# Performance work log

Measured on AMD Instinct MI355X. Metric: run time of the kernel, lower is better.

## Reference

```python
import jax, jax.numpy as jnp
import numpy as np

N_NODES = 100000
IN_C, HID_C, OUT_C = 128, 128, 64
N_EDGES, N_POS, N_NEG = 1600000, 200000, 200000
BN_EPS = 1e-5


def setup_inputs() -> dict:
    key = jax.random.key(0)
    ks = jax.random.split(key, 24)
    s = 0.05
    inp = {
        'x': jax.random.normal(ks[0], (N_NODES, IN_C), jnp.float32),
        'edge_index': jax.random.randint(ks[1], (2, N_EDGES), 0, N_NODES, jnp.int64 if jax.config.jax_enable_x64 else jnp.int32),
        'pos_edge_index': jax.random.randint(ks[2], (2, N_POS), 0, N_NODES, jnp.int32),
        'neg_edge_index': jax.random.randint(ks[3], (2, N_NEG), 0, N_NODES, jnp.int32),
        # SAGEConv layer 1 (in->hid): lin_l (bias) on aggregated neighbors, lin_r (no bias) on root
        'Wl1': jax.random.normal(ks[4], (IN_C, HID_C), jnp.float32) * s,
        'bl1': jnp.zeros((HID_C,), jnp.float32),
        'Wr1': jax.random.normal(ks[5], (IN_C, HID_C), jnp.float32) * s,
        'g1': jnp.ones((HID_C,), jnp.float32),
        'b1': jnp.zeros((HID_C,), jnp.float32),
        # SAGEConv layer 2 (hid->hid)
        'Wl2': jax.random.normal(ks[6], (HID_C, HID_C), jnp.float32) * s,
        'bl2': jnp.zeros((HID_C,), jnp.float32),
        'Wr2': jax.random.normal(ks[7], (HID_C, HID_C), jnp.float32) * s,
        'g2': jnp.ones((HID_C,), jnp.float32),
        'b2': jnp.zeros((HID_C,), jnp.float32),
        # SAGEConv layer 3 (hid->out)
        'Wl3': jax.random.normal(ks[8], (HID_C, OUT_C), jnp.float32) * s,
        'bl3': jnp.zeros((OUT_C,), jnp.float32),
        'Wr3': jax.random.normal(ks[9], (HID_C, OUT_C), jnp.float32) * s,
        # edge predictor: Linear(2*out, hid) -> ReLU -> Linear(hid, 1)
        'We1': jax.random.normal(ks[10], (2 * OUT_C, HID_C), jnp.float32) * s,
        'be1': jnp.zeros((HID_C,), jnp.float32),
        'We2': jax.random.normal(ks[11], (HID_C, 1), jnp.float32) * s,
        'be2': jnp.zeros((1,), jnp.float32),
    }
    return inp


def _sage_conv(x, src, dst, Wl, bl, Wr):
    # mean aggregation of source features at destination nodes (PyG SAGEConv default)
    msg = x[src]                                                   # [E, C] gather
    agg = jax.ops.segment_sum(msg, dst, num_segments=N_NODES)      # [N, C] scatter-add
    deg = jax.ops.segment_sum(jnp.ones((src.shape[0],), x.dtype), dst, num_segments=N_NODES)
    mean = agg / jnp.maximum(deg, 1.0)[:, None]
    return mean @ Wl + bl + x @ Wr


def _bn_eval(x, gamma, beta):
    # BatchNorm1d eval mode with init running stats (mean 0, var 1)
    return x * (gamma / jnp.sqrt(1.0 + BN_EPS)) + beta


def _encode(x, edge_index, Wl1, bl1, Wr1, g1, b1, Wl2, bl2, Wr2, g2, b2, Wl3, bl3, Wr3):
    src, dst = edge_index[0], edge_index[1]
    h = x
    # layer 1 (+ residual: in_channels == hidden_channels)
    h1 = jax.nn.relu(_bn_eval(_sage_conv(h, src, dst, Wl1, bl1, Wr1), g1, b1))
    h = h1 + h if h.shape[1] == h1.shape[1] else h1
    # layer 2 (+ residual)
    h2 = jax.nn.relu(_bn_eval(_sage_conv(h, src, dst, Wl2, bl2, Wr2), g2, b2))
    h = h2 + h
    # output layer (no norm/relu/residual)
    return _sage_conv(h, src, dst, Wl3, bl3, Wr3)


def _decode(z, edge_index, We1, be1, We2, be2):
    s, d = edge_index[0], edge_index[1]
    ef = jnp.concatenate([z[s], z[d]], axis=-1)           # [E, 2*OUT_C]
    hidden = jax.nn.relu(ef @ We1 + be1)
    return jax.nn.sigmoid((hidden @ We2 + be2)[:, 0])


def reference(x, edge_index, pos_edge_index, neg_edge_index,
              Wl1, bl1, Wr1, g1, b1, Wl2, bl2, Wr2, g2, b2, Wl3, bl3, Wr3,
              We1, be1, We2, be2):
    z = _encode(x, edge_index, Wl1, bl1, Wr1, g1, b1, Wl2, bl2, Wr2, g2, b2, Wl3, bl3, Wr3)
    pos = _decode(z, pos_edge_index, We1, be1, We2, be2)
    neg = _decode(z, neg_edge_index, We1, be1, We2, be2)
    return (z, pos, neg)
```

## Files before the change

kernel.cpp:

```cpp
#include <hip/hip_runtime.h>
#include <hip/hip_bf16.h>

typedef unsigned short u16;
typedef unsigned char u8;
typedef short short8 __attribute__((ext_vector_type(8)));
typedef float floatx4 __attribute__((ext_vector_type(4)));
typedef float floatx2 __attribute__((ext_vector_type(2)));

__device__ __forceinline__ float b2f(u16 u) {
    unsigned v = ((unsigned)u) << 16;
    float f;
    __builtin_memcpy(&f, &v, 4);
    return f;
}
__device__ __forceinline__ float b2f_lo(unsigned w) { return b2f((u16)(w & 0xffffu)); }
__device__ __forceinline__ float b2f_hi(unsigned w) { return b2f((u16)(w >> 16)); }
__device__ __forceinline__ u16 f2b(float f) {
    unsigned u;
    __builtin_memcpy(&u, &f, 4);
    u = u + 0x7fffu + ((u >> 16) & 1u);
    return (u16)(u >> 16);
}
__device__ __forceinline__ unsigned pack2(float a, float b) {
    return (unsigned)f2b(a) | ((unsigned)f2b(b) << 16);
}
__device__ __forceinline__ float loadp(const void* p, int i, int f) {
    return f ? ((const float*)p)[i] : b2f(((const u16*)p)[i]);
}
__device__ __forceinline__ u8 f2e4m3(float v) {
    int r = __builtin_amdgcn_cvt_pk_fp8_f32(v, v, 0, false);
    return (u8)(r & 0xff);
}
__device__ __forceinline__ void acc16_fp8(float* a, uint4 p) {
    floatx2 f;
    f = __builtin_amdgcn_cvt_pk_f32_fp8((int)p.x, false); a[0] += f[0];  a[1] += f[1];
    f = __builtin_amdgcn_cvt_pk_f32_fp8((int)p.x, true);  a[2] += f[0];  a[3] += f[1];
    f = __builtin_amdgcn_cvt_pk_f32_fp8((int)p.y, false); a[4] += f[0];  a[5] += f[1];
    f = __builtin_amdgcn_cvt_pk_f32_fp8((int)p.y, true);  a[6] += f[0];  a[7] += f[1];
    f = __builtin_amdgcn_cvt_pk_f32_fp8((int)p.z, false); a[8] += f[0];  a[9] += f[1];
    f = __builtin_amdgcn_cvt_pk_f32_fp8((int)p.z, true);  a[10] += f[0]; a[11] += f[1];
    f = __builtin_amdgcn_cvt_pk_f32_fp8((int)p.w, false); a[12] += f[0]; a[13] += f[1];
    f = __builtin_amdgcn_cvt_pk_f32_fp8((int)p.w, true);  a[14] += f[0]; a[15] += f[1];
}

__global__ void sniff_kernel(const unsigned* __restrict__ xw, const int* __restrict__ eiw,
                             int* __restrict__ flags) {
    __shared__ int s_fp32, s_i64;
    if (threadIdx.x == 0) { s_fp32 = 0; s_i64 = 1; }
    __syncthreads();
    int t = threadIdx.x;
    unsigned w = xw[t];
    float lo = b2f_lo(w);
    if (!(fabsf(lo) <= 64.0f)) atomicOr(&s_fp32, 1);
    if (eiw[2 * t + 1] != 0) atomicAnd(&s_i64, 0);
    __syncthreads();
    if (t == 0) { flags[0] = s_fp32; flags[1] = s_i64; }
}

__global__ void cvt_x_kernel(const void* __restrict__ x, u16* __restrict__ xb,
                             u16* __restrict__ x8,
                             const int* __restrict__ flags, int nPairs) {
    int f = flags[0];
    int i = blockIdx.x * 256 + threadIdx.x;
    if (i >= nPairs) return;
    float lo, hi;
    if (f) {
        float2 v = ((const float2*)x)[i];
        lo = v.x; hi = v.y;
        ((unsigned*)xb)[i] = pack2(lo, hi);
    } else {
        unsigned w = ((const unsigned*)x)[i];
        lo = b2f_lo(w); hi = b2f_hi(w);
        ((unsigned*)xb)[i] = w;
    }
    int r = __builtin_amdgcn_cvt_pk_fp8_f32(lo, hi, 0, false);
    x8[i] = (u16)(r & 0xffff);
}

__global__ void prep_all_kernel(const void* Wl1, const void* Wr1, u16* __restrict__ Wcat1,
                                const void* Wl2, const void* Wr2, u16* __restrict__ Wcat2,
                                const void* Wl3, const void* Wr3, u16* __restrict__ Wcat3,
                                const void* We1, u16* __restrict__ Web,
                                const void* g1, const void* b1, const void* bl1,
                                float* __restrict__ al1, float* __restrict__ bt1,
                                const void* g2, const void* b2, const void* bl2,
                                float* __restrict__ al2, float* __restrict__ bt2,
                                const void* bl3,
                                float* __restrict__ al3, float* __restrict__ bt3,
                                const void* be1, const void* We2, const void* be2,
                                float* __restrict__ dparams,
                                const int* __restrict__ flags) {
    int f = flags[0];
    int idx = blockIdx.x * 256 + threadIdx.x;
    if (idx < 16384) {
        int k = idx >> 7, n = idx & 127;
        Wcat1[n * 256 + k]       = f ? f2b(((const float*)Wl1)[idx]) : ((const u16*)Wl1)[idx];
        Wcat1[n * 256 + 128 + k] = f ? f2b(((const float*)Wr1)[idx]) : ((const u16*)Wr1)[idx];
    } else if (idx < 32768) {
        int i = idx - 16384;
        int k = i >> 7, n = i & 127;
        Wcat2[n * 256 + k]       = f ? f2b(((const float*)Wl2)[i]) : ((const u16*)Wl2)[i];
        Wcat2[n * 256 + 128 + k] = f ? f2b(((const float*)Wr2)[i]) : ((const u16*)Wr2)[i];
    } else if (idx < 49152) {
        int i = idx - 32768;
        int k = i >> 7, n = i & 127;
        const void* src = (n < 64) ? Wl3 : Wr3;
        int j = k * 64 + (n & 63);
        Wcat3[n * 128 + k] = f ? f2b(((const float*)src)[j]) : ((const u16*)src)[j];
    } else if (idx < 65536) {
        int i = idx - 49152;
        int k = i >> 7, n = i & 127;
        Web[n * 128 + k] = f ? f2b(((const float*)We1)[i]) : ((const u16*)We1)[i];
    } else {
        int i = idx - 65536;
        if (i < 128) {
            float s = loadp(g1, i, f) * rsqrtf(1.0f + 1e-5f);
            al1[i] = s;
            bt1[i] = loadp(bl1, i, f) * s + loadp(b1, i, f);
        } else if (i < 256) {
            int j = i - 128;
            float s = loadp(g2, j, f) * rsqrtf(1.0f + 1e-5f);
            al2[j] = s;
            bt2[j] = loadp(bl2, j, f) * s + loadp(b2, j, f);
        } else if (i < 384) {
            int j = i - 256;
            al3[j] = 1.0f;
            bt3[j] = (j < 64) ? 0.0f : loadp(bl3, j - 64, f);
        } else if (i < 512) {
            int j = i - 384;
            dparams[j] = loadp(be1, j, f);
            dparams[128 + j] = loadp(We2, j, f);
            if (j == 0) dparams[256] = loadp(be2, 0, f);
        }
    }
}

__device__ __forceinline__ int edge_at(const int* ei, long long idx, int i64) {
    return i64 ? ei[2 * idx] : ei[idx];
}

__global__ __launch_bounds__(256) void bucket_count_kernel(const int* __restrict__ ei,
                                                           int* __restrict__ blockhist,
                                                           int E, int EPB, int B1, int nbuck,
                                                           const int* __restrict__ flags) {
    __shared__ int hist[1024];
    for (int i = threadIdx.x; i < nbuck; i += 256) hist[i] = 0;
    __syncthreads();
    int i64 = flags[1];
    int b = blockIdx.x;
    int lo = b * EPB, hi = min(lo + EPB, E);
    for (int e = lo + (int)threadIdx.x; e < hi; e += 256) {
        int d = edge_at(ei, (long long)E + e, i64);
        atomicAdd(&hist[d >> 7], 1);
    }
    __syncthreads();
    for (int k = threadIdx.x; k < nbuck; k += 256)
        blockhist[(size_t)k * B1 + b] = hist[k];
}

__global__ __launch_bounds__(64) void colscan_kernel(int* __restrict__ blockhist,
                                                     int* __restrict__ coltot, int B1) {
    int k = blockIdx.x, l = threadIdx.x;
    int* bh = blockhist + (size_t)k * B1;
    int x0 = (l < B1) ? bh[l] : 0;
    int x1 = (64 + l < B1) ? bh[64 + l] : 0;
    int s0 = x0;
    #pragma unroll
    for (int off = 1; off < 64; off <<= 1) {
        int u = __shfl_up(s0, off, 64);
        if (l >= off) s0 += u;
    }
    int tot0 = __shfl(s0, 63, 64);
    int s1 = x1;
    #pragma unroll
    for (int off = 1; off < 64; off <<= 1) {
        int u = __shfl_up(s1, off, 64);
        if (l >= off) s1 += u;
    }
    int tot1 = __shfl(s1, 63, 64);
    s1 += tot0;
    if (l < B1) bh[l] = s0 - x0;
    if (64 + l < B1) bh[64 + l] = s1 - x1;
    if (l == 0) coltot[k] = tot0 + tot1;
}

__global__ __launch_bounds__(1024) void base_scan_kernel(const int* __restrict__ coltot,
                                                         int* __restrict__ bucketbase,
                                                         int* __restrict__ rowptrN,
                                                         int nbuck, int E) {
    __shared__ int wsum[16];
    int t = threadIdx.x, lane = t & 63, w = t >> 6;
    int v = (t < nbuck) ? coltot[t] : 0;
    int inc = v;
    #pragma unroll
    for (int off = 1; off < 64; off <<= 1) {
        int u = __shfl_up(inc, off, 64);
        if (lane >= off) inc += u;
    }
    if (lane == 63) wsum[w] = inc;
    __syncthreads();
    int add = 0;
    for (int i = 0; i < w; ++i) add += wsum[i];
    if (t < nbuck) bucketbase[t] = add + inc - v;
    if (t == 0) rowptrN[0] = E;
}

__global__ __launch_bounds__(256) void bucket_scatter_kernel(const int* __restrict__ ei,
                                                             const int* __restrict__ bucketbase,
                                                             const int* __restrict__ blockhist,
                                                             int2* __restrict__ pairs,
                                                             int E, int EPB, int B1, int nbuck,
                                                             const int* __restrict__ flags) {
    __shared__ int off[1024];
    int b = blockIdx.x;
    for (int k = threadIdx.x; k < nbuck; k += 256)
        off[k] = bucketbase[k] + blockhist[(size_t)k * B1 + b];
    __syncthreads();
    int i64 = flags[1];
    int lo = b * EPB, hi = min(lo + EPB, E);
    for (int e = lo + (int)threadIdx.x; e < hi; e += 256) {
        int s = edge_at(ei, e, i64);
        int d = edge_at(ei, (long long)E + e, i64);
        int slot = atomicAdd(&off[d >> 7], 1);
        pairs[slot] = make_int2(s, d);
    }
}

__global__ __launch_bounds__(256) void bucket_csr_kernel(const int2* __restrict__ pairs,
                                                         const int* __restrict__ bucketbase,
                                                         const int* __restrict__ coltot,
                                                         int* __restrict__ rowptr,
                                                         int* __restrict__ col, int N) {
    __shared__ int srcs[4096];
    __shared__ unsigned char dl[4096];
    __shared__ int hist[128], cur[128];
    int k = blockIdx.x, tid = threadIdx.x;
    if (tid < 128) hist[tid] = 0;
    __syncthreads();
    int base = bucketbase[k], cnt = coltot[k];
    int staged = min(cnt, 4096);
    for (int i = tid; i < cnt; i += 256) {
        int2 pr = pairs[base + i];
        int j = pr.y & 127;
        atomicAdd(&hist[j], 1);
        if (i < 4096) { srcs[i] = pr.x; dl[i] = (unsigned char)j; }
    }
    __syncthreads();
    if (tid < 64) {
        int x0 = hist[tid], x1 = hist[64 + tid];
        int s0 = x0;
        #pragma unroll
        for (int off = 1; off < 64; off <<= 1) {
            int u = __shfl_up(s0, off, 64);
            if (tid >= off) s0 += u;
        }
        int tot0 = __shfl(s0, 63, 64);
        int s1 = x1;
        #pragma unroll
        for (int off = 1; off < 64; off <<= 1) {
            int u = __shfl_up(s1, off, 64);
            if (tid >= off) s1 += u;
        }
        s1 += tot0;
        cur[tid] = s0 - x0;
        cur[64 + tid] = s1 - x1;
    }
    __syncthreads();
    int node0 = k << 7;
    if (tid < 128 && node0 + tid < N) rowptr[node0 + tid] = base + cur[tid];
    __syncthreads();
    for (int i = tid; i < staged; i += 256) {
        int slot = base + atomicAdd(&cur[dl[i]], 1);
        col[slot] = srcs[i];
    }
    for (int i = 4096 + tid; i < cnt; i += 256) {
        int2 pr = pairs[base + i];
        int slot = base + atomicAdd(&cur[pr.y & 127], 1);
        col[slot] = pr.x;
    }
}

template <int CH>
__global__ __launch_bounds__(256) void aggregate_fp8_kernel(const u8* __restrict__ X8,
                                                            const int* __restrict__ rowptr,
                                                            const int* __restrict__ col,
                                                            u16* __restrict__ meanout, int N) {
    constexpr int LPR = CH / 16;
    constexpr int GPB = 256 / LPR;
    int t = threadIdx.x;
    int g = t / LPR;
    int o = t % LPR;
    int u = blockIdx.x * GPB + g;
    if (u >= N) return;
    const uint4* Xv = (const uint4*)X8;
    int beg = rowptr[u], end = rowptr[u + 1];
    float a[16];
    #pragma unroll
    for (int i = 0; i < 16; ++i) a[i] = 0.f;
    int e = beg;
    for (; e + 8 <= end; e += 8) {
        uint4 p0 = Xv[(size_t)col[e]     * LPR + o];
        uint4 p1 = Xv[(size_t)col[e + 1] * LPR + o];
        uint4 p2 = Xv[(size_t)col[e + 2] * LPR + o];
        uint4 p3 = Xv[(size_t)col[e + 3] * LPR + o];
        uint4 p4 = Xv[(size_t)col[e + 4] * LPR + o];
        uint4 p5 = Xv[(size_t)col[e + 5] * LPR + o];
        uint4 p6 = Xv[(size_t)col[e + 6] * LPR + o];
        uint4 p7 = Xv[(size_t)col[e + 7] * LPR + o];
        acc16_fp8(a, p0); acc16_fp8(a, p1); acc16_fp8(a, p2); acc16_fp8(a, p3);
        acc16_fp8(a, p4); acc16_fp8(a, p5); acc16_fp8(a, p6); acc16_fp8(a, p7);
    }
    for (; e + 4 <= end; e += 4) {
        uint4 p0 = Xv[(size_t)col[e]     * LPR + o];
        uint4 p1 = Xv[(size_t)col[e + 1] * LPR + o];
        uint4 p2 = Xv[(size_t)col[e + 2] * LPR + o];
        uint4 p3 = Xv[(size_t)col[e + 3] * LPR + o];
        acc16_fp8(a, p0); acc16_fp8(a, p1); acc16_fp8(a, p2); acc16_fp8(a, p3);
    }
    for (; e < end; ++e) {
        uint4 p = Xv[(size_t)col[e] * LPR + o];
        acc16_fp8(a, p);
    }
    int deg = end - beg;
    float inv = (deg > 0) ? 1.0f / (float)deg : 0.0f;
    uint4 ov0, ov1;
    ov0.x = pack2(a[0] * inv, a[1] * inv);   ov0.y = pack2(a[2] * inv, a[3] * inv);
    ov0.z = pack2(a[4] * inv, a[5] * inv);   ov0.w = pack2(a[6] * inv, a[7] * inv);
    ov1.x = pack2(a[8] * inv, a[9] * inv);   ov1.y = pack2(a[10] * inv, a[11] * inv);
    ov1.z = pack2(a[12] * inv, a[13] * inv); ov1.w = pack2(a[14] * inv, a[15] * inv);
    uint4* mo = (uint4*)meanout;
    mo[(size_t)u * (CH / 8) + o * 2 + 0] = ov0;
    mo[(size_t)u * (CH / 8) + o * 2 + 1] = ov1;
}

__global__ __launch_bounds__(256) void agg_combine_kernel(const u8* __restrict__ T8,
                                                          const int* __restrict__ rowptr,
                                                          const int* __restrict__ col,
                                                          const u16* __restrict__ ubuf,
                                                          u16* __restrict__ zbuf,
                                                          void* __restrict__ dout,
                                                          int N, const int* __restrict__ flags) {
    constexpr int LPR = 4;
    constexpr int GPB = 64;
    int f = flags[0];
    int t = threadIdx.x;
    int g = t / LPR;
    int o = t % LPR;
    int u = blockIdx.x * GPB + g;
    if (u >= N) return;
    const uint4* Xv = (const uint4*)T8;
    int beg = rowptr[u], end = rowptr[u + 1];
    float a[16];
    #pragma unroll
    for (int i = 0; i < 16; ++i) a[i] = 0.f;
    int e = beg;
    for (; e + 8 <= end; e += 8) {
        uint4 p0 = Xv[(size_t)col[e]     * LPR + o];
        uint4 p1 = Xv[(size_t)col[e + 1] * LPR + o];
        uint4 p2 = Xv[(size_t)col[e + 2] * LPR + o];
        uint4 p3 = Xv[(size_t)col[e + 3] * LPR + o];
        uint4 p4 = Xv[(size_t)col[e + 4] * LPR + o];
        uint4 p5 = Xv[(size_t)col[e + 5] * LPR + o];
        uint4 p6 = Xv[(size_t)col[e + 6] * LPR + o];
        uint4 p7 = Xv[(size_t)col[e + 7] * LPR + o];
        acc16_fp8(a, p0); acc16_fp8(a, p1); acc16_fp8(a, p2); acc16_fp8(a, p3);
        acc16_fp8(a, p4); acc16_fp8(a, p5); acc16_fp8(a, p6); acc16_fp8(a, p7);
    }
    for (; e + 4 <= end; e += 4) {
        uint4 p0 = Xv[(size_t)col[e]     * LPR + o];
        uint4 p1 = Xv[(size_t)col[e + 1] * LPR + o];
        uint4 p2 = Xv[(size_t)col[e + 2] * LPR + o];
        uint4 p3 = Xv[(size_t)col[e + 3] * LPR + o];
        acc16_fp8(a, p0); acc16_fp8(a, p1); acc16_fp8(a, p2); acc16_fp8(a, p3);
    }
    for (; e < end; ++e) {
        uint4 p = Xv[(size_t)col[e] * LPR + o];
        acc16_fp8(a, p);
    }
    int deg = end - beg;
    float inv = (deg > 0) ? 1.0f / (float)deg : 0.0f;
    const uint4* uv = (const uint4*)(ubuf + (size_t)u * 64 + o * 16);
    uint4 u0 = uv[0], u1 = uv[1];
    float z[16];
    z[0] = a[0] * inv + b2f_lo(u0.x);  z[1] = a[1] * inv + b2f_hi(u0.x);
    z[2] = a[2] * inv + b2f_lo(u0.y);  z[3] = a[3] * inv + b2f_hi(u0.y);
    z[4] = a[4] * inv + b2f_lo(u0.z);  z[5] = a[5] * inv + b2f_hi(u0.z);
    z[6] = a[6] * inv + b2f_lo(u0.w);  z[7] = a[7] * inv + b2f_hi(u0.w);
    z[8] = a[8] * inv + b2f_lo(u1.x);  z[9] = a[9] * inv + b2f_hi(u1.x);
    z[10] = a[10] * inv + b2f_lo(u1.y); z[11] = a[11] * inv + b2f_hi(u1.y);
    z[12] = a[12] * inv + b2f_lo(u1.z); z[13] = a[13] * inv + b2f_hi(u1.z);
    z[14] = a[14] * inv + b2f_lo(u1.w); z[15] = a[15] * inv + b2f_hi(u1.w);
    uint4 zv0, zv1;
    zv0.x = pack2(z[0], z[1]);   zv0.y = pack2(z[2], z[3]);
    zv0.z = pack2(z[4], z[5]);   zv0.w = pack2(z[6], z[7]);
    zv1.x = pack2(z[8], z[9]);   zv1.y = pack2(z[10], z[11]);
    zv1.z = pack2(z[12], z[13]); zv1.w = pack2(z[14], z[15]);
    uint4* zo = (uint4*)(zbuf + (size_t)u * 64 + o * 16);
    zo[0] = zv0; zo[1] = zv1;
    if (f) {
        float* fo = (float*)dout + (size_t)u * 64 + o * 16;
        #pragma unroll
        for (int i = 0; i < 16; ++i) fo[i] = z[i];
    } else {
        uint4* bo = (uint4*)((u16*)dout + (size_t)u * 64 + o * 16);
        bo[0] = zv0; bo[1] = zv1;
    }
}

#define LDSA 40
__global__ __launch_bounds__(256) void gemm_sage_kernel(
    const u16* __restrict__ A1, const u16* __restrict__ A2,
    const u16* __restrict__ WT,
    const float* __restrict__ alpha, const float* __restrict__ beta,
    int addRes, u16* __restrict__ out, int ldo, u16* __restrict__ outB,
    u8* __restrict__ out8, int ld8,
    int M, int K, int relu) {
    __shared__ u16 As[64 * LDSA];
    int tid = threadIdx.x;
    int mBase = blockIdx.x * 64;
    int lane = tid & 63, w = tid >> 6;
    int wm = w >> 1, wn = w & 1;
    int q = lane >> 4, r = lane & 15;

    floatx4 acc[2][4];
    #pragma unroll
    for (int mi = 0; mi < 2; ++mi)
        #pragma unroll
        for (int ni = 0; ni < 4; ++ni)
            acc[mi][ni] = (floatx4){0.f, 0.f, 0.f, 0.f};

    int arow = tid >> 2, akc = (tid & 3) * 8;
    int agr = mBase + arow;

    const u16* wr[4];
    #pragma unroll
    for (int ni = 0; ni < 4; ++ni)
        wr[ni] = WT + (size_t)(wn * 64 + ni * 16 + r) * K + q * 8;

    short8 bcur[4];
    #pragma unroll
    for (int ni = 0; ni < 4; ++ni) bcur[ni] = *(const short8*)(wr[ni]);

    short8 acur = (short8){0, 0, 0, 0, 0, 0, 0, 0};
    if (agr < M) acur = *(const short8*)(A1 + (size_t)agr * 128 + akc);

    for (int k0 = 0; k0 < K; k0 += 32) {
        *(short8*)(&As[arow * LDSA + akc]) = acur;
        int k1 = k0 + 32;
        short8 anxt = acur;
        short8 bnxt[4];
        #pragma unroll
        for (int ni = 0; ni < 4; ++ni) bnxt[ni] = bcur[ni];
        if (k1 < K) {
            const u16* Ab = (k1 < 128) ? (A1 + k1) : (A2 + (k1 - 128));
            if (agr < M) anxt = *(const short8*)(Ab + (size_t)agr * 128 + akc);
            #pragma unroll
            for (int ni = 0; ni < 4; ++ni) bnxt[ni] = *(const short8*)(wr[ni] + k1);
        }
        __syncthreads();
        short8 af[2];
        #pragma unroll
        for (int mi = 0; mi < 2; ++mi)
            af[mi] = *(const short8*)(&As[(wm * 32 + mi * 16 + r) * LDSA + q * 8]);
        #pragma unroll
        for (int mi = 0; mi < 2; ++mi)
            #pragma unroll
            for (int ni = 0; ni < 4; ++ni)
                acc[mi][ni] = __builtin_amdgcn_mfma_f32_16x16x32_bf16(af[mi], bcur[ni], acc[mi][ni], 0, 0, 0);
        __syncthreads();
        acur = anxt;
        #pragma unroll
        for (int ni = 0; ni < 4; ++ni) bcur[ni] = bnxt[ni];
    }

    #pragma unroll
    for (int mi = 0; mi < 2; ++mi)
        #pragma unroll
        for (int ni = 0; ni < 4; ++ni) {
            int colv = wn * 64 + ni * 16 + r;
            float al = alpha[colv], be = beta[colv];
            #pragma unroll
            for (int r4 = 0; r4 < 4; ++r4) {
                int row = mBase + wm * 32 + mi * 16 + q * 4 + r4;
                if (row < M) {
                    float v = acc[mi][ni][r4] * al + be;
                    if (relu) v = fmaxf(v, 0.0f);
                    if (addRes) v += b2f(A2[(size_t)row * 128 + colv]);
                    if (outB) {
                        if (colv < 64) out8[(size_t)row * 64 + colv] = f2e4m3(v);
                        else outB[(size_t)row * 64 + (colv - 64)] = f2b(v);
                    } else {
                        out[(size_t)row * ldo + colv] = f2b(v);
                        if (out8) out8[(size_t)row * ld8 + colv] = f2e4m3(v);
                    }
                }
            }
        }
}

__global__ __launch_bounds__(256) void decode_kernel(
    const u16* __restrict__ z,
    const int* __restrict__ pos, const int* __restrict__ neg,
    int nPos, int nNeg, int blocksPos,
    const u16* __restrict__ WebT,
    const float* __restrict__ dparams,
    void* __restrict__ dout, long long posBase,
    const int* __restrict__ flags) {
    __shared__ u16 As[64 * 136];
    __shared__ float red[4][32];
    __shared__ float be1f[128], We2f[128];
    int tid = threadIdx.x;
    int f = flags[0];
    int b = blockIdx.x;
    const int* sidx; const int* didx; int nE; long long outBase; int eBase;
    if (b < blocksPos) {
        sidx = pos; didx = pos + nPos; nE = nPos; outBase = posBase; eBase = b * 64;
    } else {
        sidx = neg; didx = neg + nNeg; nE = nNeg; outBase = posBase + nPos;
        eBase = (b - blocksPos) * 64;
    }

    if (tid < 128) { be1f[tid] = dparams[tid]; We2f[tid] = dparams[128 + tid]; }

    {
        int row = tid >> 2, ch = tid & 3;
        int e = eBase + row;
        if (e >= nE) e = nE - 1;
        int node = (ch < 2) ? sidx[e] : didx[e];
        int off = (ch & 1) * 32;
        const short8* src = (const short8*)(z + (size_t)node * 64 + off);
        #pragma unroll
        for (int j = 0; j < 4; ++j)
            *(short8*)(&As[row * 136 + ch * 32 + j * 8]) = src[j];
    }
    __syncthreads();

    int lane = tid & 63, w = tid >> 6;
    int wm = w >> 1, wn = w & 1;
    int q = lane >> 4, r = lane & 15;
    floatx4 acc[2][4];
    #pragma unroll
    for (int mi = 0; mi < 2; ++mi)
        #pragma unroll
        for (int ni = 0; ni < 4; ++ni)
            acc[mi][ni] = (floatx4){0.f, 0.f, 0.f, 0.f};

    #pragma unroll
    for (int k0 = 0; k0 < 128; k0 += 32) {
        short8 af[2], bfv[4];
        #pragma unroll
        for (int mi = 0; mi < 2; ++mi)
            af[mi] = *(const short8*)(&As[(wm * 32 + mi * 16 + r) * 136 + k0 + q * 8]);
        #pragma unroll
        for (int ni = 0; ni < 4; ++ni)
            bfv[ni] = *(const short8*)(WebT + (size_t)(wn * 64 + ni * 16 + r) * 128 + k0 + q * 8);
        #pragma unroll
        for (int mi = 0; mi < 2; ++mi)
            #pragma unroll
            for (int ni = 0; ni < 4; ++ni)
                acc[mi][ni] = __builtin_amdgcn_mfma_f32_16x16x32_bf16(af[mi], bfv[ni], acc[mi][ni], 0, 0, 0);
    }

    float part[2][4] = {{0.f, 0.f, 0.f, 0.f}, {0.f, 0.f, 0.f, 0.f}};
    #pragma unroll
    for (int mi = 0; mi < 2; ++mi)
        #pragma unroll
        for (int ni = 0; ni < 4; ++ni) {
            int colv = wn * 64 + ni * 16 + r;
            float bb = be1f[colv], mm = We2f[colv];
            #pragma unroll
            for (int r4 = 0; r4 < 4; ++r4) {
                float v = acc[mi][ni][r4] + bb;
                part[mi][r4] += fmaxf(v, 0.0f) * mm;
            }
        }
    #pragma unroll
    for (int mi = 0; mi < 2; ++mi)
        #pragma unroll
        for (int r4 = 0; r4 < 4; ++r4) {
            float v = part[mi][r4];
            v += __shfl_xor(v, 1, 64);
            v += __shfl_xor(v, 2, 64);
            v += __shfl_xor(v, 4, 64);
            v += __shfl_xor(v, 8, 64);
            part[mi][r4] = v;
        }
    if (r == 0) {
        #pragma unroll
        for (int mi = 0; mi < 2; ++mi)
            #pragma unroll
            for (int r4 = 0; r4 < 4; ++r4)
                red[w][mi * 16 + q * 4 + r4] = part[mi][r4];
    }
    __syncthreads();
    if (tid < 64) {
        int e = eBase + tid;
        if (e < nE) {
            int half = tid >> 5, loc = tid & 31;
            float s = red[half * 2 + 0][loc] + red[half * 2 + 1][loc] + dparams[256];
            float sg = 1.0f / (1.0f + expf(-s));
            if (f) ((float*)dout)[outBase + e] = sg;
            else   ((u16*)dout)[outBase + e] = f2b(sg);
        }
    }
}


extern "C" void kernel_launch(void* const* d_in, const int* in_sizes, int n_in,
                              void* d_out, int out_size, void* d_ws, size_t ws_size,
                              hipStream_t stream) {
    const void* x   = d_in[0];
    const int* ei   = (const int*)d_in[1];
    const int* pos  = (const int*)d_in[2];
    const int* neg  = (const int*)d_in[3];
    const void* Wl1 = d_in[4];
    const void* bl1 = d_in[5];
    const void* Wr1 = d_in[6];
    const void* g1  = d_in[7];
    const void* b1  = d_in[8];
    const void* Wl2 = d_in[9];
    const void* bl2 = d_in[10];
    const void* Wr2 = d_in[11];
    const void* g2  = d_in[12];
    const void* b2  = d_in[13];
    const void* Wl3 = d_in[14];
    const void* bl3 = d_in[15];
    const void* Wr3 = d_in[16];
    const void* We1 = d_in[17];
    const void* be1 = d_in[18];
    const void* We2 = d_in[19];
    const void* be2 = d_in[20];

    const int N = in_sizes[0] / 128;
    const int E = in_sizes[1] / 2;
    const int nPos = in_sizes[2] / 2;
    const int nNeg = in_sizes[3] / 2;
    const int nbuck = (N + 127) >> 7;
    const int EPB = (((E + 95) / 96) + 3) & ~3;
    const int B1 = (E + EPB - 1) / EPB;

    char* p = (char*)d_ws;
    auto alloc = [&](size_t bytes) -> void* {
        void* r = (void*)p;
        p += (bytes + 255) & ~(size_t)255;
        return r;
    };
    int*   flags     = (int*)alloc(64);
    int*   blockhist = (int*)alloc((size_t)nbuck * B1 * 4);
    int*   coltot    = (int*)alloc((size_t)nbuck * 4);
    int*   bucketbase= (int*)alloc((size_t)nbuck * 4);
    int*   rowptr    = (int*)alloc((size_t)(N + 1) * 4);
    int2*  pairs     = (int2*)alloc((size_t)E * 8);
    int*   colbuf    = (int*)alloc((size_t)E * 4);
    u16*   xb      = (u16*)alloc((size_t)N * 128 * 2);
    u16*   hbufA   = (u16*)alloc((size_t)N * 128 * 2);
    u16*   meanbuf = (u16*)alloc((size_t)N * 128 * 2);
    u8*    x8      = (u8*)alloc((size_t)N * 128);
    u8*    h8      = (u8*)alloc((size_t)N * 128);
    u8*    t8      = (u8*)alloc((size_t)N * 64);
    u16*   Wcat1   = (u16*)alloc((size_t)256 * 128 * 2);
    u16*   Wcat2   = (u16*)alloc((size_t)256 * 128 * 2);
    u16*   Wcat3   = (u16*)alloc((size_t)128 * 128 * 2);
    u16*   Web     = (u16*)alloc((size_t)128 * 128 * 2);
    float* al1 = (float*)alloc(128 * 4);
    float* bt1 = (float*)alloc(128 * 4);
    float* al2 = (float*)alloc(128 * 4);
    float* bt2 = (float*)alloc(128 * 4);
    float* al3 = (float*)alloc(128 * 4);
    float* bt3 = (float*)alloc(128 * 4);
    float* dparams = (float*)alloc(260 * 4);
    u16* hbufB = xb;
    u16* ubuf  = meanbuf + (size_t)N * 64;
    u16* zbuf  = hbufA + (size_t)N * 64;

    sniff_kernel<<<1, 256, 0, stream>>>((const unsigned*)x, ei, flags);
    bucket_count_kernel<<<B1, 256, 0, stream>>>(ei, blockhist, E, EPB, B1, nbuck, flags);
    colscan_kernel<<<nbuck, 64, 0, stream>>>(blockhist, coltot, B1);
    base_scan_kernel<<<1, 1024, 0, stream>>>(coltot, bucketbase, rowptr + N, nbuck, E);
    bucket_scatter_kernel<<<B1, 256, 0, stream>>>(ei, bucketbase, blockhist, pairs, E, EPB, B1, nbuck, flags);
    bucket_csr_kernel<<<nbuck, 256, 0, stream>>>(pairs, bucketbase, coltot, rowptr, colbuf, N);

    cvt_x_kernel<<<(N * 64 + 255) / 256, 256, 0, stream>>>(x, xb, (u16*)x8, flags, N * 64);
    prep_all_kernel<<<(66048 + 255) / 256, 256, 0, stream>>>(
        Wl1, Wr1, Wcat1, Wl2, Wr2, Wcat2, Wl3, Wr3, Wcat3, We1, Web,
        g1, b1, bl1, al1, bt1, g2, b2, bl2, al2, bt2, bl3, al3, bt3,
        be1, We2, be2, dparams, flags);

    int gB = (N + 63) / 64;

    aggregate_fp8_kernel<128><<<(N + 31) / 32, 256, 0, stream>>>(x8, rowptr, colbuf, meanbuf, N);
    gemm_sage_kernel<<<gB, 256, 0, stream>>>(meanbuf, xb, Wcat1, al1, bt1,
                                             1, hbufA, 128, nullptr, h8, 128, N, 256, 1);
    aggregate_fp8_kernel<128><<<(N + 31) / 32, 256, 0, stream>>>(h8, rowptr, colbuf, meanbuf, N);
    gemm_sage_kernel<<<gB, 256, 0, stream>>>(meanbuf, hbufA, Wcat2, al2, bt2,
                                             1, hbufB, 128, nullptr, nullptr, 0, N, 256, 1);
    gemm_sage_kernel<<<gB, 256, 0, stream>>>(hbufB, hbufB, Wcat3, al3, bt3,
                                             0, nullptr, 0, ubuf, t8, 64, N, 128, 0);
    agg_combine_kernel<<<(N + 63) / 64, 256, 0, stream>>>(t8, rowptr, colbuf, ubuf, zbuf,
                                                          d_out, N, flags);

    long long posBase = (long long)N * 64;
    int bP = (nPos + 63) / 64, bN = (nNeg + 63) / 64;
    decode_kernel<<<bP + bN, 256, 0, stream>>>(zbuf, pos, neg, nPos, nNeg, bP,
                                               Web, dparams, d_out, posBase, flags);
}
```

Measured before the change: 517.9 us.

## Stage full A tile in LDS once and split GEMM warps along N

The SAGE GEMM now loads the whole 64xK A tile into dynamic shared memory with a single barrier, replacing the per-K-step double-buffered staging that needed two barriers per iteration. Each wave now covers all 64 rows and a 32-column slice, instead of a 2x2 warp grid. The decode kernel gets the same warp remapping, issues its z gathers and preloads the weight fragments into registers before the LDS store, and reduces across four waves. This cuts barrier count and overlaps gather latency with the weight loads, at the cost of more LDS per block, less overlap between loads and MFMA in the GEMM, and more registers.

```diff
diff --git a/kernel.cpp b/kernel.cpp
--- a/kernel.cpp
+++ b/kernel.cpp
@@ -407,7 +407,6 @@
     }
 }
 
-#define LDSA 40
 __global__ __launch_bounds__(256) void gemm_sage_kernel(
     const u16* __restrict__ A1, const u16* __restrict__ A2,
     const u16* __restrict__ WT,
@@ -415,73 +414,62 @@
     int addRes, u16* __restrict__ out, int ldo, u16* __restrict__ outB,
     u8* __restrict__ out8, int ld8,
     int M, int K, int relu) {
-    __shared__ u16 As[64 * LDSA];
+    extern __shared__ u16 As[];
+    const int stride = K + 8;
     int tid = threadIdx.x;
     int mBase = blockIdx.x * 64;
     int lane = tid & 63, w = tid >> 6;
-    int wm = w >> 1, wn = w & 1;
     int q = lane >> 4, r = lane & 15;
 
-    floatx4 acc[2][4];
-    #pragma unroll
-    for (int mi = 0; mi < 2; ++mi)
-        #pragma unroll
-        for (int ni = 0; ni < 4; ++ni)
+    {
+        int row = tid >> 2, cb = (tid & 3) * 8;
+        int gr = mBase + row;
+        for (int j = 0; j < K; j += 32) {
+            int k = cb + j;
+            short8 v = (short8){0, 0, 0, 0, 0, 0, 0, 0};
+            if (gr < M) {
+                const u16* src = (k < 128) ? (A1 + (size_t)gr * 128 + k)
+                                           : (A2 + (size_t)gr * 128 + (k - 128));
+                v = *(const short8*)src;
+            }
+            *(short8*)(&As[row * stride + k]) = v;
+        }
+    }
+    __syncthreads();
+
+    floatx4 acc[4][2];
+    #pragma unroll
+    for (int mi = 0; mi < 4; ++mi)
+        #pragma unroll
+        for (int ni = 0; ni < 2; ++ni)
             acc[mi][ni] = (floatx4){0.f, 0.f, 0.f, 0.f};
 
-    int arow = tid >> 2, akc = (tid & 3) * 8;
-    int agr = mBase + arow;
-
-    const u16* wr[4];
-    #pragma unroll
-    for (int ni = 0; ni < 4; ++ni)
-        wr[ni] = WT + (size_t)(wn * 64 + ni * 16 + r) * K + q * 8;
-
-    short8 bcur[4];
-    #pragma unroll
-    for (int ni = 0; ni < 4; ++ni) bcur[ni] = *(const short8*)(wr[ni]);
-
-    short8 acur = (short8){0, 0, 0, 0, 0, 0, 0, 0};
-    if (agr < M) acur = *(const short8*)(A1 + (size_t)agr * 128 + akc);
+    const u16* wr0 = WT + (size_t)(w * 32 + r) * K + q * 8;
+    const u16* wr1 = WT + (size_t)(w * 32 + 16 + r) * K + q * 8;
 
     for (int k0 = 0; k0 < K; k0 += 32) {
-        *(short8*)(&As[arow * LDSA + akc]) = acur;
-        int k1 = k0 + 32;
-        short8 anxt = acur;
-        short8 bnxt[4];
-        #pragma unroll
-        for (int ni = 0; ni < 4; ++ni) bnxt[ni] = bcur[ni];
-        if (k1 < K) {
-            const u16* Ab = (k1 < 128) ? (A1 + k1) : (A2 + (k1 - 128));
-            if (agr < M) anxt = *(const short8*)(Ab + (size_t)agr * 128 + akc);
-            #pragma unroll
-            for (int ni = 0; ni < 4; ++ni) bnxt[ni] = *(const short8*)(wr[ni] + k1);
-        }
-        __syncthreads();
-        short8 af[2];
-        #pragma unroll
-        for (int mi = 0; mi < 2; ++mi)
-            af[mi] = *(const short8*)(&As[(wm * 32 + mi * 16 + r) * LDSA + q * 8]);
-        #pragma unroll
-        for (int mi = 0; mi < 2; ++mi)
-            #pragma unroll
-            for (int ni = 0; ni < 4; ++ni)
-                acc[mi][ni] = __builtin_amdgcn_mfma_f32_16x16x32_bf16(af[mi], bcur[ni], acc[mi][ni], 0, 0, 0);
-        __syncthreads();
-        acur = anxt;
-        #pragma unroll
-        for (int ni = 0; ni < 4; ++ni) bcur[ni] = bnxt[ni];
-    }
-
-    #pragma unroll
-    for (int mi = 0; mi < 2; ++mi)
-        #pragma unroll
-        for (int ni = 0; ni < 4; ++ni) {
-            int colv = wn * 64 + ni * 16 + r;
+        short8 b0 = *(const short8*)(wr0 + k0);
+        short8 b1 = *(const short8*)(wr1 + k0);
+        short8 af[4];
+        #pragma unroll
+        for (int mi = 0; mi < 4; ++mi)
+            af[mi] = *(const short8*)(&As[(mi * 16 + r) * stride + k0 + q * 8]);
+        #pragma unroll
+        for (int mi = 0; mi < 4; ++mi) {
+            acc[mi][0] = __builtin_amdgcn_mfma_f32_16x16x32_bf16(af[mi], b0, acc[mi][0], 0, 0, 0);
+            acc[mi][1] = __builtin_amdgcn_mfma_f32_16x16x32_bf16(af[mi], b1, acc[mi][1], 0, 0, 0);
+        }
+    }
+
+    #pragma unroll
+    for (int mi = 0; mi < 4; ++mi)
+        #pragma unroll
+        for (int ni = 0; ni < 2; ++ni) {
+            int colv = w * 32 + ni * 16 + r;
             float al = alpha[colv], be = beta[colv];
             #pragma unroll
             for (int r4 = 0; r4 < 4; ++r4) {
-                int row = mBase + wm * 32 + mi * 16 + q * 4 + r4;
+                int row = mBase + mi * 16 + q * 4 + r4;
                 if (row < M) {
                     float v = acc[mi][ni][r4] * al + be;
                     if (relu) v = fmaxf(v, 0.0f);
@@ -507,7 +495,7 @@
     void* __restrict__ dout, long long posBase,
     const int* __restrict__ flags) {
     __shared__ u16 As[64 * 136];
-    __shared__ float red[4][32];
+    __shared__ float red[4][64];
     __shared__ float be1f[128], We2f[128];
     int tid = threadIdx.x;
     int f = flags[0];
@@ -520,8 +508,10 @@
         eBase = (b - blocksPos) * 64;
     }
 
-    if (tid < 128) { be1f[tid] = dparams[tid]; We2f[tid] = dparams[128 + tid]; }
-
+    int lane = tid & 63, w = tid >> 6;
+    int q = lane >> 4, r = lane & 15;
+
+    short8 zr[4];
     {
         int row = tid >> 2, ch = tid & 3;
         int e = eBase + row;
@@ -530,43 +520,60 @@
         int off = (ch & 1) * 32;
         const short8* src = (const short8*)(z + (size_t)node * 64 + off);
         #pragma unroll
+        for (int j = 0; j < 4; ++j) zr[j] = src[j];
+    }
+
+    if (tid < 128) { be1f[tid] = dparams[tid]; We2f[tid] = dparams[128 + tid]; }
+
+    short8 bfw[4][2];
+    {
+        const u16* w0 = WebT + (size_t)(w * 32 + r) * 128 + q * 8;
+        const u16* w1 = WebT + (size_t)(w * 32 + 16 + r) * 128 + q * 8;
+        #pragma unroll
+        for (int kk = 0; kk < 4; ++kk) {
+            bfw[kk][0] = *(const short8*)(w0 + kk * 32);
+            bfw[kk][1] = *(const short8*)(w1 + kk * 32);
+        }
+    }
+
+    {
+        int row = tid >> 2, ch = tid & 3;
+        #pragma unroll
         for (int j = 0; j < 4; ++j)
-            *(short8*)(&As[row * 136 + ch * 32 + j * 8]) = src[j];
-    }
-    __syncthreads();
-
-    int lane = tid & 63, w = tid >> 6;
-    int wm = w >> 1, wn = w & 1;
-    int q = lane >> 4, r = lane & 15;
-    floatx4 acc[2][4];
-    #pragma unroll
-    for (int mi = 0; mi < 2; ++mi)
-        #pragma unroll
-        for (int ni = 0; ni < 4; ++ni)
+            *(short8*)(&As[row * 136 + ch * 32 + j * 8]) = zr[j];
+    }
+    __syncthreads();
+
+    floatx4 acc[4][2];
+    #pragma unroll
+    for (int mi = 0; mi < 4; ++mi)
+        #pragma unroll
+        for (int ni = 0; ni < 2; ++ni)
             acc[mi][ni] = (floatx4){0.f, 0.f, 0.f, 0.f};
 
     #pragma unroll
-    for (int k0 = 0; k0 < 128; k0 += 32) {
-        short8 af[2], bfv[4];
-        #pragma unroll
-        for (int mi = 0; mi < 2; ++mi)
-            af[mi] = *(const short8*)(&As[(wm * 32 + mi * 16 + r) * 136 + k0 + q * 8]);
-        #pragma unroll
-        for (int ni = 0; ni < 4; ++ni)
-            bfv[ni] = *(const short8*)(WebT + (size_t)(wn * 64 + ni * 16 + r) * 128 + k0 + q * 8);
-        #pragma unroll
-        for (int mi = 0; mi < 2; ++mi)
-            #pragma unroll
-            for (int ni = 0; ni < 4; ++ni)
-                acc[mi][ni] = __builtin_amdgcn_mfma_f32_16x16x32_bf16(af[mi], bfv[ni], acc[mi][ni], 0, 0, 0);
-    }
-
-    float part[2][4] = {{0.f, 0.f, 0.f, 0.f}, {0.f, 0.f, 0.f, 0.f}};
-    #pragma unroll
-    for (int mi = 0; mi < 2; ++mi)
-        #pragma unroll
-        for (int ni = 0; ni < 4; ++ni) {
-            int colv = wn * 64 + ni * 16 + r;
+    for (int kk = 0; kk < 4; ++kk) {
+        short8 af[4];
+        #pragma unroll
+        for (int mi = 0; mi < 4; ++mi)
+            af[mi] = *(const short8*)(&As[(mi * 16 + r) * 136 + kk * 32 + q * 8]);
+        #pragma unroll
+        for (int mi = 0; mi < 4; ++mi) {
+            acc[mi][0] = __builtin_amdgcn_mfma_f32_16x16x32_bf16(af[mi], bfw[kk][0], acc[mi][0], 0, 0, 0);
+            acc[mi][1] = __builtin_amdgcn_mfma_f32_16x16x32_bf16(af[mi], bfw[kk][1], acc[mi][1], 0, 0, 0);
+        }
+    }
+
+    float part[4][4];
+    #pragma unroll
+    for (int mi = 0; mi < 4; ++mi)
+        #pragma unroll
+        for (int r4 = 0; r4 < 4; ++r4) part[mi][r4] = 0.f;
+    #pragma unroll
+    for (int mi = 0; mi < 4; ++mi)
+        #pragma unroll
+        for (int ni = 0; ni < 2; ++ni) {
+            int colv = w * 32 + ni * 16 + r;
             float bb = be1f[colv], mm = We2f[colv];
             #pragma unroll
             for (int r4 = 0; r4 < 4; ++r4) {
@@ -575,7 +582,7 @@
             }
         }
     #pragma unroll
-    for (int mi = 0; mi < 2; ++mi)
+    for (int mi = 0; mi < 4; ++mi)
         #pragma unroll
         for (int r4 = 0; r4 < 4; ++r4) {
             float v = part[mi][r4];
@@ -587,7 +594,7 @@
         }
     if (r == 0) {
         #pragma unroll
-        for (int mi = 0; mi < 2; ++mi)
+        for (int mi = 0; mi < 4; ++mi)
             #pragma unroll
             for (int r4 = 0; r4 < 4; ++r4)
                 red[w][mi * 16 + q * 4 + r4] = part[mi][r4];
@@ -596,8 +603,7 @@
     if (tid < 64) {
         int e = eBase + tid;
         if (e < nE) {
-            int half = tid >> 5, loc = tid & 31;
-            float s = red[half * 2 + 0][loc] + red[half * 2 + 1][loc] + dparams[256];
+            float s = red[0][tid] + red[1][tid] + red[2][tid] + red[3][tid] + dparams[256];
             float sg = 1.0f / (1.0f + expf(-s));
             if (f) ((float*)dout)[outBase + e] = sg;
             else   ((u16*)dout)[outBase + e] = f2b(sg);
@@ -687,15 +693,17 @@
         be1, We2, be2, dparams, flags);
 
     int gB = (N + 63) / 64;
+    size_t lds256 = (size_t)64 * (256 + 8) * 2;
+    size_t lds128 = (size_t)64 * (128 + 8) * 2;
 
     aggregate_fp8_kernel<128><<<(N + 31) / 32, 256, 0, stream>>>(x8, rowptr, colbuf, meanbuf, N);
-    gemm_sage_kernel<<<gB, 256, 0, stream>>>(meanbuf, xb, Wcat1, al1, bt1,
-                                             1, hbufA, 128, nullptr, h8, 128, N, 256, 1);
+    gemm_sage_kernel<<<gB, 256, lds256, stream>>>(meanbuf, xb, Wcat1, al1, bt1,
+                                                  1, hbufA, 128, nullptr, h8, 128, N, 256, 1);
     aggregate_fp8_kernel<128><<<(N + 31) / 32, 256, 0, stream>>>(h8, rowptr, colbuf, meanbuf, N);
-    gemm_sage_kernel<<<gB, 256, 0, stream>>>(meanbuf, hbufA, Wcat2, al2, bt2,
-                                             1, hbufB, 128, nullptr, nullptr, 0, N, 256, 1);
-    gemm_sage_kernel<<<gB, 256, 0, stream>>>(hbufB, hbufB, Wcat3, al3, bt3,
-                                             0, nullptr, 0, ubuf, t8, 64, N, 128, 0);
+    gemm_sage_kernel<<<gB, 256, lds256, stream>>>(meanbuf, hbufA, Wcat2, al2, bt2,
+                                                  1, hbufB, 128, nullptr, nullptr, 0, N, 256, 1);
+    gemm_sage_kernel<<<gB, 256, lds128, stream>>>(hbufB, hbufB, Wcat3, al3, bt3,
+                                                  0, nullptr, 0, ubuf, t8, 64, N, 128, 0);
     agg_combine_kernel<<<(N + 63) / 64, 256, 0, stream>>>(t8, rowptr, colbuf, ubuf, zbuf,
                                                           d_out, N, flags);
 
```

New measurement: 490.6 us. 5.3% less time.
